# Performance work log

Measured on AMD Instinct MI355X. Metric: run time of the kernel, lower is better.

The kernel has to match this reference:

```python
import jax, jax.numpy as jnp
import numpy as np

BATCH_SIZE = 512   # number of molecules (init kwarg)
D_FEAT = 512       # atom feature dim
N_ATOMS = 65536    # total atoms across the ragged batch


def setup_inputs() -> dict:
    # Deterministic ragged segment sizes: each molecule gets >=1 atom, sum == N_ATOMS.
    rng = np.random.default_rng(0)
    counts = rng.multinomial(N_ATOMS - BATCH_SIZE, np.full(BATCH_SIZE, 1.0 / BATCH_SIZE)) + 1
    molecule_indicator = np.repeat(np.arange(BATCH_SIZE), counts)  # sorted segment ids, [N]
    key = jax.random.key(0)
    atom_features = jax.random.normal(key, (N_ATOMS, D_FEAT), dtype=jnp.float32)
    return {
        "atom_features": atom_features,
        "molecule_indicator": jnp.asarray(molecule_indicator, dtype=jnp.int32),
    }


def reference(atom_features, molecule_indicator):
    n, d = atom_features.shape
    # Per-molecule atom counts via one segment-sum (replaces the O(B*N) mask loop).
    counts = jax.ops.segment_sum(jnp.ones(n, jnp.int32), molecule_indicator,
                                 num_segments=BATCH_SIZE)
    starts = jnp.cumsum(counts) - counts                      # exclusive prefix sum
    pos = jnp.arange(n) - starts[molecule_indicator]          # within-molecule position
    max_atoms = int(counts.max())                             # dynamic pad length (eager)
    # Single O(N) scatter: ragged rows -> dense [B, max_atoms, D] (zeros == padding).
    dense = jnp.zeros((BATCH_SIZE, max_atoms, d), atom_features.dtype)
    dense = dense.at[molecule_indicator, pos].set(atom_features)
    # Original drops batch rows whose total sum is exactly 0 (i.e. empty molecules).
    keep_idx = jnp.nonzero(jnp.sum(dense, axis=(1, 2)) != 0)[0]
    return jnp.take(dense, keep_idx, axis=0)
```

## Files before the change

### kernel.cpp

```cpp
#include <hip/hip_runtime.h>


#define BATCH 512
#define UNROLL 8

typedef float f32x4 __attribute__((ext_vector_type(4)));

__global__ void find_starts_kernel(const int* __restrict__ mol, int n,
                                   int* __restrict__ starts, int batch) {
    int i = blockIdx.x * blockDim.x + threadIdx.x;
    if (i >= n) return;
    if (i == 0) {
        starts[mol[0]] = 0;
        starts[batch] = n;
    } else if (mol[i] != mol[i - 1]) {
        starts[mol[i]] = i;
    }
}

__global__ void gather_pad_kernel(const f32x4* __restrict__ in,
                                  const int* __restrict__ starts,
                                  f32x4* __restrict__ out,
                                  int row4) {
    const int m = blockIdx.y;
    const int s = starts[m];
    const int cnt = starts[m + 1] - s;
    const f32x4* __restrict__ inm = in + (long long)s * 128;
    f32x4* __restrict__ outm = out + (long long)m * row4;

    int j = blockIdx.x * (blockDim.x * UNROLL) + threadIdx.x;
    #pragma unroll
    for (int u = 0; u < UNROLL; ++u, j += 256) {
        if (j < row4) {
            const int a = j >> 7;
            f32x4 v = (f32x4)(0.f);
            if (a < cnt) v = inm[j];
            __builtin_nontemporal_store(v, &outm[j]);
        }
    }
}

extern "C" void kernel_launch(void* const* d_in, const int* in_sizes, int n_in,
                              void* d_out, int out_size, void* d_ws, size_t ws_size,
                              hipStream_t stream) {
    const float* atom_features = (const float*)d_in[0];
    const int* mol = (const int*)d_in[1];
    float* out = (float*)d_out;

    const int n = in_sizes[1];
    const int d = in_sizes[0] / n;
    const int max_atoms = out_size / (BATCH * d);
    const int d4 = d / 4;
    const int row4 = max_atoms * d4;

    int* starts = (int*)d_ws;

    find_starts_kernel<<<(n + 255) / 256, 256, 0, stream>>>(mol, n, starts, BATCH);

    dim3 grid((row4 + 256 * UNROLL - 1) / (256 * UNROLL), BATCH);
    gather_pad_kernel<<<grid, 256, 0, stream>>>(
        (const f32x4*)atom_features, starts, (f32x4*)out, row4);
}
```

Measured before the change: 54.26 us.

## Fuse segment-start computation into gather kernel via per-block binary search

Drops the separate find_starts kernel. Each gather block now binary-searches the sorted molecule ids in global memory to find its segment start and end. Full blocks also skip the per-element bounds check. This removes one kernel launch and the dependency between the two kernels, but every block pays about 16 dependent global loads before it can start streaming.

```diff
diff --git a/kernel.cpp b/kernel.cpp
--- a/kernel.cpp
+++ b/kernel.cpp
@@ -3,39 +3,53 @@
 
 #define BATCH 512
 #define UNROLL 8
+#define TPB 256
 
 typedef float f32x4 __attribute__((ext_vector_type(4)));
 
-__global__ void find_starts_kernel(const int* __restrict__ mol, int n,
-                                   int* __restrict__ starts, int batch) {
-    int i = blockIdx.x * blockDim.x + threadIdx.x;
-    if (i >= n) return;
-    if (i == 0) {
-        starts[mol[0]] = 0;
-        starts[batch] = n;
-    } else if (mol[i] != mol[i - 1]) {
-        starts[mol[i]] = i;
+__global__ void gather_pad_fused(const f32x4* __restrict__ in,
+                                 const int* __restrict__ mol,
+                                 f32x4* __restrict__ out,
+                                 int n, int row4, int nxfull) {
+    const int m = blockIdx.y;
+
+    __shared__ int sh[2];
+    if (threadIdx.x < 2) {
+        const int target = m + threadIdx.x;
+        int lo = 0, hi = n;
+        while (lo < hi) {
+            const int mid = (lo + hi) >> 1;
+            if (mol[mid] < target) lo = mid + 1; else hi = mid;
+        }
+        sh[threadIdx.x] = lo;
     }
-}
+    __syncthreads();
+    const int s = sh[0];
+    const int cnt = sh[1] - sh[0];
 
-__global__ void gather_pad_kernel(const f32x4* __restrict__ in,
-                                  const int* __restrict__ starts,
-                                  f32x4* __restrict__ out,
-                                  int row4) {
-    const int m = blockIdx.y;
-    const int s = starts[m];
-    const int cnt = starts[m + 1] - s;
     const f32x4* __restrict__ inm = in + (long long)s * 128;
     f32x4* __restrict__ outm = out + (long long)m * row4;
 
-    int j = blockIdx.x * (blockDim.x * UNROLL) + threadIdx.x;
-    #pragma unroll
-    for (int u = 0; u < UNROLL; ++u, j += 256) {
-        if (j < row4) {
+    const int j0 = blockIdx.x * (TPB * UNROLL) + threadIdx.x;
+    if (blockIdx.x < nxfull) {
+        #pragma unroll
+        for (int u = 0; u < UNROLL; ++u) {
+            const int j = j0 + u * TPB;
             const int a = j >> 7;
             f32x4 v = (f32x4)(0.f);
             if (a < cnt) v = inm[j];
             __builtin_nontemporal_store(v, &outm[j]);
+        }
+    } else {
+        #pragma unroll
+        for (int u = 0; u < UNROLL; ++u) {
+            const int j = j0 + u * TPB;
+            if (j < row4) {
+                const int a = j >> 7;
+                f32x4 v = (f32x4)(0.f);
+                if (a < cnt) v = inm[j];
+                __builtin_nontemporal_store(v, &outm[j]);
+            }
         }
     }
 }
@@ -53,11 +67,11 @@
     const int d4 = d / 4;
     const int row4 = max_atoms * d4;
 
-    int* starts = (int*)d_ws;
+    const int span = TPB * UNROLL;
+    const int nx = (row4 + span - 1) / span;
+    const int nxfull = row4 / span;
 
-    find_starts_kernel<<<(n + 255) / 256, 256, 0, stream>>>(mol, n, starts, BATCH);
-
-    dim3 grid((row4 + 256 * UNROLL - 1) / (256 * UNROLL), BATCH);
-    gather_pad_kernel<<<grid, 256, 0, stream>>>(
-        (const f32x4*)atom_features, starts, (f32x4*)out, row4);
+    dim3 grid(nx, BATCH);
+    gather_pad_fused<<<grid, TPB, 0, stream>>>(
+        (const f32x4*)atom_features, mol, (f32x4*)out, n, row4, nxfull);
 }
```

New measurement: 54.33 us. Within noise of the previous version (+0.1%).
